# Kernel tuning notes

Hardware: AMD Instinct MI355X
Metric: run time of the kernel (lower is better)

Reference implementation:

```python
import jax, jax.numpy as jnp
import numpy as np

B, D, N = 8, 512, 4096
HEADS, DH = 8, 64
HID = HEADS * DH  # 512
SCALE = DH ** -0.5


def setup_inputs() -> dict:
    key = jax.random.key(0)
    k0, k1, k2, k3 = jax.random.split(key, 4)
    x = jax.random.normal(k0, (B, D, N), dtype=jnp.float32)
    w_qkv = jax.random.normal(k1, (3 * HID, D), dtype=jnp.float32) * 0.02
    w_out = jax.random.normal(k2, (D, HID), dtype=jnp.float32) * 0.02
    b_out = jax.random.normal(k3, (D,), dtype=jnp.float32) * 0.02
    g = jnp.ones((1, D, 1), dtype=jnp.float32)
    return {"x": x, "w_qkv": w_qkv, "w_out": w_out, "b_out": b_out, "g": g}


def reference(x, w_qkv, w_out, b_out, g):
    # 1x1 Conv1d (no bias) == channel matmul: [b, 3*HID, n]
    qkv = jnp.einsum('od,bdn->bon', w_qkv, x)
    q, k, v = jnp.split(qkv, 3, axis=1)
    # b (h c) n -> b h c n
    q = q.reshape(B, HEADS, DH, N)
    k = k.reshape(B, HEADS, DH, N)
    v = v.reshape(B, HEADS, DH, N)
    q = jax.nn.softmax(q, axis=2) * SCALE  # softmax over feature dim d
    k = jax.nn.softmax(k, axis=3)          # softmax over sequence dim n
    context = jnp.einsum('bhdn,bhen->bhde', k, v)   # [b,h,d,e]
    out = jnp.einsum('bhde,bhdn->bhen', context, q)  # [b,h,e,n]
    out = out.reshape(B, HID, N)
    # 1x1 Conv1d with bias
    y = jnp.einsum('oh,bhn->bon', w_out, out) + b_out[None, :, None]
    # RMSNorm: F.normalize(y, dim=1) * g * sqrt(D)
    norm = jnp.sqrt(jnp.sum(y * y, axis=1, keepdims=True))
    y = y / jnp.maximum(norm, 1e-12) * g * jnp.asarray(D, y.dtype) ** 0.5
    return y
```

## Files before the change

kernel.cpp:

```cpp
#include <hip/hip_runtime.h>
#include <math.h>

#define B 8
#define D 512
#define N 4096
#define HEADS 8
#define DH 64
#define HID 512
#define O3 1536
#define KDIM 512
#define SCALE 0.125f
#define SQRT_D 22.62741699796952f

typedef __attribute__((ext_vector_type(4))) float f32x4;
typedef __attribute__((ext_vector_type(8))) short bf16x8;

static __device__ __forceinline__ unsigned short f2bf(float f) {
    unsigned int u = __float_as_uint(f);
    unsigned int r = (u + 0x7fffu + ((u >> 16) & 1u)) >> 16;
    return (unsigned short)r;
}

static __device__ __forceinline__ float bf2f(unsigned short u) {
    return __uint_as_float((unsigned int)u << 16);
}

static __device__ __forceinline__ void gload_lds16(const void* g, void* l) {
    __builtin_amdgcn_global_load_lds(
        (const __attribute__((address_space(1))) unsigned int*)g,
        (__attribute__((address_space(3))) unsigned int*)l, 16, 0, 0);
}

__global__ __launch_bounds__(256) void cvt_w(const float* __restrict__ w,
                                             unsigned short* __restrict__ wb) {
    int i = (blockIdx.x * 256 + threadIdx.x) * 4;
    float4 v = *(const float4*)(w + i);
    __align__(8) unsigned short o[4] = {f2bf(v.x), f2bf(v.y), f2bf(v.z), f2bf(v.w)};
    *(uint2*)(wb + i) = *(const uint2*)o;
}

__global__ __launch_bounds__(256) void transpose_x(const float* __restrict__ x,
                                                   unsigned short* __restrict__ xT) {
    __shared__ float tile[64][65];
    const int n0 = blockIdx.x * 64, d0 = blockIdx.y * 64, b = blockIdx.z;
    const float* xb = x + (size_t)b * D * N;
    unsigned short* xTb = xT + (size_t)b * N * KDIM;
    const int t = threadIdx.x;
    const int r = t >> 4, c4 = (t & 15) * 4;
#pragma unroll
    for (int i = 0; i < 4; ++i) {
        int row = r + i * 16;
        float4 v = *(const float4*)(xb + (size_t)(d0 + row) * N + n0 + c4);
        tile[row][c4 + 0] = v.x;
        tile[row][c4 + 1] = v.y;
        tile[row][c4 + 2] = v.z;
        tile[row][c4 + 3] = v.w;
    }
    __syncthreads();
#pragma unroll
    for (int pass = 0; pass < 2; ++pass) {
        int orow = (t >> 3) + pass * 32;
        int oc = (t & 7) * 8;
        __align__(16) unsigned short o[8];
#pragma unroll
        for (int e = 0; e < 8; ++e) o[e] = f2bf(tile[oc + e][orow]);
        *(uint4*)(xTb + (size_t)(n0 + orow) * KDIM + d0 + oc) = *(const uint4*)o;
    }
}

#define GEMM_CORE(A_PTR, BT_PTR, ACC)                                              \
    __shared__ __align__(16) unsigned short As[128 * 64];                          \
    __shared__ __align__(16) unsigned short Bs[128 * 64];                          \
    const int t = threadIdx.x;                                                     \
    const int lane = t & 63;                                                       \
    const int wid = t >> 6;                                                        \
    const int wm = wid >> 1, wn = wid & 1;                                         \
    int prow[4], coff[4];                                                          \
    _Pragma("unroll") for (int i = 0; i < 4; ++i) {                                \
        int p = i * 4096 + t * 16;                                                 \
        int pr = p >> 7;                                                           \
        int pc = (p >> 4) & 7;                                                     \
        prow[i] = pr;                                                              \
        coff[i] = (pc ^ (pr & 7)) * 8;                                             \
    }                                                                              \
    int aoff[4][2], boff[4][2];                                                    \
    _Pragma("unroll") for (int m = 0; m < 4; ++m) {                                \
        int arow = wm * 64 + m * 16 + (lane & 15);                                 \
        int brow = wn * 64 + m * 16 + (lane & 15);                                 \
        _Pragma("unroll") for (int s = 0; s < 2; ++s) {                            \
            int chunk = s * 4 + (lane >> 4);                                       \
            aoff[m][s] = arow * 128 + ((chunk ^ (arow & 7)) << 4);                 \
            boff[m][s] = brow * 128 + ((chunk ^ (brow & 7)) << 4);                 \
        }                                                                          \
    }                                                                              \
    f32x4 ACC[4][4] = {};                                                          \
    for (int k0 = 0; k0 < KDIM; k0 += 64) {                                        \
        _Pragma("unroll") for (int i = 0; i < 4; ++i)                              \
            gload_lds16(A_PTR + (size_t)(row0 + prow[i]) * KDIM + k0 + coff[i],    \
                        (char*)As + i * 4096 + t * 16);                            \
        _Pragma("unroll") for (int i = 0; i < 4; ++i)                              \
            gload_lds16(BT_PTR + (size_t)(col0 + prow[i]) * KDIM + k0 + coff[i],   \
                        (char*)Bs + i * 4096 + t * 16);                            \
        __syncthreads();                                                           \
        bf16x8 af[4][2], bfr[4][2];                                                \
        _Pragma("unroll") for (int m = 0; m < 4; ++m)                              \
            _Pragma("unroll") for (int s = 0; s < 2; ++s) {                        \
                af[m][s] = *(const bf16x8*)((const char*)As + aoff[m][s]);         \
                bfr[m][s] = *(const bf16x8*)((const char*)Bs + boff[m][s]);        \
            }                                                                      \
        _Pragma("unroll") for (int s = 0; s < 2; ++s)                              \
            _Pragma("unroll") for (int m = 0; m < 4; ++m)                          \
                _Pragma("unroll") for (int n = 0; n < 4; ++n)                      \
                    ACC[m][n] = __builtin_amdgcn_mfma_f32_16x16x32_bf16(           \
                        af[m][s], bfr[n][s], ACC[m][n], 0, 0, 0);                  \
        __syncthreads();                                                           \
    }

__global__ __launch_bounds__(256) void gemm_kv(const unsigned short* __restrict__ Aw,
                                               const unsigned short* __restrict__ BTall,
                                               unsigned short* __restrict__ kvall) {
    const int b = blockIdx.z;
    const unsigned short* A = Aw;
    const unsigned short* BT = BTall + (size_t)b * N * KDIM;
    unsigned short* C = kvall + (size_t)b * 1024 * N;
    const int row0 = blockIdx.y * 128;
    const int col0 = blockIdx.x * 128;
    GEMM_CORE(A, BT, acc)
#pragma unroll
    for (int m = 0; m < 4; ++m) {
        int row_b = row0 + wm * 64 + m * 16 + (lane >> 4) * 4;
#pragma unroll
        for (int n = 0; n < 4; ++n) {
            int col = col0 + wn * 64 + n * 16 + (lane & 15);
#pragma unroll
            for (int r = 0; r < 4; ++r)
                C[(size_t)(row_b + r) * N + col] = f2bf(acc[m][n][r]);
        }
    }
}

__global__ __launch_bounds__(256) void gemm_q_sm(const unsigned short* __restrict__ Aw,
                                                 const unsigned short* __restrict__ BTall,
                                                 unsigned short* __restrict__ qT) {
    const int b = blockIdx.z;
    const unsigned short* A = Aw;
    const unsigned short* BT = BTall + (size_t)b * N * KDIM;
    const int row0 = blockIdx.y * 128;
    const int col0 = blockIdx.x * 128;
    GEMM_CORE(A, BT, acc)
    const int h = blockIdx.y * 2 + wm;
    const int g = lane >> 4;
#pragma unroll
    for (int nf = 0; nf < 4; ++nf) {
        float mx = -1e30f;
#pragma unroll
        for (int m = 0; m < 4; ++m)
#pragma unroll
            for (int r = 0; r < 4; ++r) mx = fmaxf(mx, acc[m][nf][r]);
        mx = fmaxf(mx, __shfl_xor(mx, 16));
        mx = fmaxf(mx, __shfl_xor(mx, 32));
        float e[16];
        float s = 0.f;
#pragma unroll
        for (int m = 0; m < 4; ++m)
#pragma unroll
            for (int r = 0; r < 4; ++r) {
                e[m * 4 + r] = __expf(acc[m][nf][r] - mx);
                s += e[m * 4 + r];
            }
        s += __shfl_xor(s, 16);
        s += __shfl_xor(s, 32);
        float rs = SCALE / s;
        int n = col0 + wn * 64 + nf * 16 + (lane & 15);
        unsigned short* dst = qT + ((size_t)b * N + n) * KDIM + h * 64 + g * 4;
#pragma unroll
        for (int m = 0; m < 4; ++m) {
            __align__(8) unsigned short o4[4] = {f2bf(e[m * 4 + 0] * rs), f2bf(e[m * 4 + 1] * rs),
                                                 f2bf(e[m * 4 + 2] * rs), f2bf(e[m * 4 + 3] * rs)};
            *(uint2*)(dst + m * 16) = *(const uint2*)o4;
        }
    }
}

__global__ __launch_bounds__(256) void context_mfma3(const unsigned short* __restrict__ kvb,
                                                     float* __restrict__ ctx,
                                                     float* __restrict__ ksum) {
    const int ch = blockIdx.x, h = blockIdx.y, b = blockIdx.z;
    const int K0 = ch * 512;
    const unsigned short* kbase = kvb + ((size_t)b * 1024 + h * DH) * (size_t)N + K0;
    const unsigned short* vbase = kvb + ((size_t)b * 1024 + 512 + h * DH) * (size_t)N + K0;

    __shared__ __align__(16) unsigned short Ks[64 * 64];
    __shared__ __align__(16) unsigned short Vs[64 * 64];

    const int t = threadIdx.x;
    const int lane = t & 63;
    const int wv = t >> 6;

    const int kr = t >> 2;
    const int kc = (t & 3) * 16;
    const int kchunk0 = kc >> 3;
    const int kdst0 = kr * 128 + (((kchunk0 + 0) ^ (kr & 7)) << 4);
    const int kdst1 = kr * 128 + (((kchunk0 + 1) ^ (kr & 7)) << 4);

    int vrow[2], vcoff[2];
#pragma unroll
    for (int i = 0; i < 2; ++i) {
        int p = i * 4096 + t * 16;
        int pr = p >> 7;
        int pc = (p >> 4) & 7;
        vrow[i] = pr;
        vcoff[i] = (pc ^ (pr & 7)) * 8;
    }

    const int ar = wv * 16 + (lane & 15);
    int aoff[2], boff[4][2];
#pragma unroll
    for (int s = 0; s < 2; ++s) {
        int chunk = s * 4 + (lane >> 4);
        aoff[s] = ar * 128 + ((chunk ^ (ar & 7)) << 4);
#pragma unroll
        for (int nf = 0; nf < 4; ++nf) {
            int br = nf * 16 + (lane & 15);
            boff[nf][s] = br * 128 + ((chunk ^ (br & 7)) << 4);
        }
    }

    bf16x8 ones;
#pragma unroll
    for (int j = 0; j < 8; ++j) ones[j] = (short)0x3F80;

    f32x4 acc[4] = {};
    f32x4 accs = {};

    for (int k0 = 0; k0 < 512; k0 += 64) {
#pragma unroll
        for (int i = 0; i < 2; ++i)
            gload_lds16(vbase + (size_t)vrow[i] * N + k0 + vcoff[i],
                        (char*)Vs + i * 4096 + t * 16);
        __align__(16) unsigned short raw[16];
        *(uint4*)raw = *(const uint4*)(kbase + (size_t)kr * N + k0 + kc);
        *(uint4*)(raw + 8) = *(const uint4*)(kbase + (size_t)kr * N + k0 + kc + 8);
        __align__(16) unsigned short o[16];
#pragma unroll
        for (int j = 0; j < 16; ++j) o[j] = f2bf(__expf(bf2f(raw[j])));
        *(uint4*)((char*)Ks + kdst0) = *(const uint4*)o;
        *(uint4*)((char*)Ks + kdst1) = *(const uint4*)(o + 8);
        __syncthreads();

        bf16x8 av[2], bv[4][2];
#pragma unroll
        for (int s = 0; s < 2; ++s) {
            av[s] = *(const bf16x8*)((const char*)Ks + aoff[s]);
#pragma unroll
            for (int nf = 0; nf < 4; ++nf)
                bv[nf][s] = *(const bf16x8*)((const char*)Vs + boff[nf][s]);
        }
#pragma unroll
        for (int s = 0; s < 2; ++s) {
#pragma unroll
            for (int nf = 0; nf < 4; ++nf)
                acc[nf] = __builtin_amdgcn_mfma_f32_16x16x32_bf16(av[s], bv[nf][s], acc[nf], 0, 0, 0);
            accs = __builtin_amdgcn_mfma_f32_16x16x32_bf16(av[s], ones, accs, 0, 0, 0);
        }
        __syncthreads();
    }

    float* cbase = ctx + ((size_t)(b * HEADS + h)) * DH * DH;
    const int drow = wv * 16 + (lane >> 4) * 4;
#pragma unroll
    for (int nf = 0; nf < 4; ++nf) {
        int e = nf * 16 + (lane & 15);
#pragma unroll
        for (int rr = 0; rr < 4; ++rr)
            atomicAdd(&cbase[(drow + rr) * DH + e], acc[nf][rr]);
    }
    if ((lane & 15) == 0) {
#pragma unroll
        for (int rr = 0; rr < 4; ++rr)
            atomicAdd(&ksum[b * 512 + h * DH + drow + rr], accs[rr]);
    }
}

__global__ __launch_bounds__(256) void fold_wout3(const float* __restrict__ w_out,
                                                  const float* __restrict__ ctx,
                                                  const float* __restrict__ ksum,
                                                  unsigned short* __restrict__ w2) {
    const int ot = blockIdx.x, h = blockIdx.y, b = blockIdx.z;
    __shared__ __align__(16) unsigned short As[128 * 64];
    __shared__ __align__(16) unsigned short Bs[64 * 64];
    const int t = threadIdx.x;
    const int lane = t & 63;
    const int wv = t >> 6;

#pragma unroll
    for (int i = 0; i < 8; ++i) {
        int lin = t + i * 256;
        int r = lin >> 4;
        int c4 = (lin & 15) * 4;
        float4 v = *(const float4*)(w_out + (size_t)(ot * 128 + r) * HID + h * 64 + c4);
        __align__(8) unsigned short o4[4] = {f2bf(v.x), f2bf(v.y), f2bf(v.z), f2bf(v.w)};
        int chunk = c4 >> 3;
        int off = (c4 & 7) * 2;
        *(uint2*)((char*)As + r * 128 + ((chunk ^ (r & 7)) << 4) + off) = *(const uint2*)o4;
    }
    const float* cb = ctx + ((size_t)(b * HEADS + h)) * DH * DH;
    const float* ks = ksum + b * 512 + h * 64;
#pragma unroll
    for (int i = 0; i < 4; ++i) {
        int lin = t + i * 256;
        int r = lin >> 4;
        int c4 = (lin & 15) * 4;
        float inv = 1.0f / ks[r];
        float4 v = *(const float4*)(cb + (size_t)r * DH + c4);
        __align__(8) unsigned short o4[4] = {f2bf(v.x * inv), f2bf(v.y * inv),
                                             f2bf(v.z * inv), f2bf(v.w * inv)};
        int chunk = c4 >> 3;
        int off = (c4 & 7) * 2;
        *(uint2*)((char*)Bs + r * 128 + ((chunk ^ (r & 7)) << 4) + off) = *(const uint2*)o4;
    }
    __syncthreads();

    f32x4 acc[2][4] = {};
#pragma unroll
    for (int s = 0; s < 2; ++s) {
        int chunk = s * 4 + (lane >> 4);
        bf16x8 bf[4];
#pragma unroll
        for (int nf = 0; nf < 4; ++nf) {
            int brow = nf * 16 + (lane & 15);
            bf[nf] = *(const bf16x8*)((const char*)Bs + brow * 128 + ((chunk ^ (brow & 7)) << 4));
        }
#pragma unroll
        for (int mm = 0; mm < 2; ++mm) {
            int arow = (wv * 2 + mm) * 16 + (lane & 15);
            bf16x8 a = *(const bf16x8*)((const char*)As + arow * 128 + ((chunk ^ (arow & 7)) << 4));
#pragma unroll
            for (int nf = 0; nf < 4; ++nf)
                acc[mm][nf] = __builtin_amdgcn_mfma_f32_16x16x32_bf16(a, bf[nf], acc[mm][nf], 0, 0, 0);
        }
    }

#pragma unroll
    for (int mm = 0; mm < 2; ++mm) {
        int o_base = ot * 128 + (wv * 2 + mm) * 16 + (lane >> 4) * 4;
#pragma unroll
        for (int nf = 0; nf < 4; ++nf) {
            int d = nf * 16 + (lane & 15);
#pragma unroll
            for (int rr = 0; rr < 4; ++rr)
                w2[((size_t)(b * D) + o_base + rr) * D + h * 64 + d] = f2bf(acc[mm][nf][rr]);
        }
    }
}

__global__ __launch_bounds__(256) void gemm_y(const unsigned short* __restrict__ w2all,
                                              const unsigned short* __restrict__ qTall,
                                              const float* __restrict__ bias,
                                              float* __restrict__ yall,
                                              float* __restrict__ colsum) {
    const int b = blockIdx.z;
    const unsigned short* A = w2all + (size_t)b * D * D;
    const unsigned short* BT = qTall + (size_t)b * N * KDIM;
    float* y = yall + (size_t)b * D * N;
    const int row0 = blockIdx.y * 128;
    const int col0 = blockIdx.x * 128;
    GEMM_CORE(A, BT, acc)

    float csum[4] = {0.f, 0.f, 0.f, 0.f};
#pragma unroll
    for (int m = 0; m < 4; ++m) {
        int row_b = row0 + wm * 64 + m * 16 + (lane >> 4) * 4;
#pragma unroll
        for (int r = 0; r < 4; ++r) {
            float bv = bias[row_b + r];
#pragma unroll
            for (int n = 0; n < 4; ++n) {
                int col = col0 + wn * 64 + n * 16 + (lane & 15);
                float e = acc[m][n][r] + bv;
                y[(size_t)(row_b + r) * N + col] = e;
                csum[n] += e * e;
            }
        }
    }
#pragma unroll
    for (int n = 0; n < 4; ++n) {
        csum[n] += __shfl_xor(csum[n], 16);
        csum[n] += __shfl_xor(csum[n], 32);
    }
    if (lane < 16) {
#pragma unroll
        for (int n = 0; n < 4; ++n) {
            int col = col0 + wn * 64 + n * 16 + lane;
            atomicAdd(&colsum[b * N + col], csum[n]);
        }
    }
}

__global__ __launch_bounds__(256) void colprep(float* __restrict__ cs) {
    int i = blockIdx.x * 256 + threadIdx.x;
    float v = cs[i];
    cs[i] = SQRT_D / fmaxf(sqrtf(v), 1e-12f);
}

__global__ __launch_bounds__(256) void rmsnorm4(float4* __restrict__ y,
                                                const float4* __restrict__ rinv,
                                                const float* __restrict__ g) {
    const size_t total = (size_t)B * D * N / 4;
    for (size_t i = blockIdx.x * 256 + threadIdx.x; i < total; i += 524288) {
        int b = (int)(i >> 19);
        int rem = (int)(i & 524287);
        int o = rem >> 10;
        int n4 = rem & 1023;
        float4 v = y[i];
        float4 rv = rinv[b * 1024 + n4];
        float go = g[o];
        v.x *= rv.x * go;
        v.y *= rv.y * go;
        v.z *= rv.z * go;
        v.w *= rv.w * go;
        y[i] = v;
    }
}

extern "C" void kernel_launch(void* const* d_in, const int* in_sizes, int n_in,
                              void* d_out, int out_size, void* d_ws, size_t ws_size,
                              hipStream_t stream) {
    const float* x = (const float*)d_in[0];
    const float* w_qkv = (const float*)d_in[1];
    const float* w_out = (const float*)d_in[2];
    const float* b_out = (const float*)d_in[3];
    const float* g = (const float*)d_in[4];
    float* out = (float*)d_out;

    unsigned short* kvb = (unsigned short*)d_ws;
    float* ctx = (float*)(kvb + (size_t)B * 1024 * N);
    float* ksum = ctx + (size_t)B * HEADS * DH * DH;
    float* colsum = ksum + B * 512;
    unsigned short* w2 = (unsigned short*)(colsum + B * N);
    unsigned short* wqb = w2 + (size_t)B * D * D;
    unsigned short* xT = wqb + (size_t)O3 * KDIM;
    unsigned short* qT = xT + (size_t)B * N * KDIM;

    hipMemsetAsync(ctx, 0,
                   ((size_t)B * HEADS * DH * DH + B * 512 + B * N) * sizeof(float), stream);

    cvt_w<<<dim3(O3 * KDIM / 1024), 256, 0, stream>>>(w_qkv, wqb);
    transpose_x<<<dim3(N / 64, D / 64, B), 256, 0, stream>>>(x, xT);

    gemm_q_sm<<<dim3(N / 128, HID / 128, B), 256, 0, stream>>>(wqb, xT, qT);
    gemm_kv<<<dim3(N / 128, 8, B), 256, 0, stream>>>(wqb + (size_t)HID * KDIM, xT, kvb);

    context_mfma3<<<dim3(8, HEADS, B), 256, 0, stream>>>(kvb, ctx, ksum);
    fold_wout3<<<dim3(4, HEADS, B), 256, 0, stream>>>(w_out, ctx, ksum, w2);

    gemm_y<<<dim3(N / 128, D / 128, B), 256, 0, stream>>>(w2, qT, b_out, out, colsum);

    colprep<<<dim3(B * N / 256), 256, 0, stream>>>(colsum);
    rmsnorm4<<<dim3(2048), 256, 0, stream>>>((float4*)out, (const float4*)colsum, g);
}
```

Before: 172.2 us.

## Double-buffer GEMM LDS tiles and merge Q and KV projection GEMMs

Makes the shared GEMM core double-buffered in LDS: it prefetches the next K tile while computing on the current one, with one barrier per iteration instead of two. It also merges the separate Q-softmax and KV projection GEMM launches into one gemm_qkv kernel whose blocks pick the epilogue from blockIdx.y. The aim is to hide global-to-LDS latency and to drop a launch plus tail effects. In exchange LDS use per block doubles to 64KB, which can lower occupancy.

```diff
diff --git a/kernel.cpp b/kernel.cpp
--- a/kernel.cpp
+++ b/kernel.cpp
@@ -68,9 +68,17 @@
     }
 }
 
-#define GEMM_CORE(A_PTR, BT_PTR, ACC)                                              \
-    __shared__ __align__(16) unsigned short As[128 * 64];                          \
-    __shared__ __align__(16) unsigned short Bs[128 * 64];                          \
+#define STAGE_AB(A_PTR, BT_PTR, BUFOFF, KOFF)                                      \
+    _Pragma("unroll") for (int i = 0; i < 4; ++i)                                  \
+        gload_lds16(A_PTR + (size_t)(row0 + prow[i]) * KDIM + (KOFF) + coff[i],    \
+                    (char*)As + (BUFOFF) + i * 4096 + t * 16);                     \
+    _Pragma("unroll") for (int i = 0; i < 4; ++i)                                  \
+        gload_lds16(BT_PTR + (size_t)(col0 + prow[i]) * KDIM + (KOFF) + coff[i],   \
+                    (char*)Bs + (BUFOFF) + i * 4096 + t * 16);
+
+#define GEMM_CORE_DB(A_PTR, BT_PTR, ACC)                                           \
+    __shared__ __align__(16) unsigned short As[2 * 128 * 64];                      \
+    __shared__ __align__(16) unsigned short Bs[2 * 128 * 64];                      \
     const int t = threadIdx.x;                                                     \
     const int lane = t & 63;                                                       \
     const int wid = t >> 6;                                                        \
@@ -94,19 +102,18 @@
         }                                                                          \
     }                                                                              \
     f32x4 ACC[4][4] = {};                                                          \
-    for (int k0 = 0; k0 < KDIM; k0 += 64) {                                        \
-        _Pragma("unroll") for (int i = 0; i < 4; ++i)                              \
-            gload_lds16(A_PTR + (size_t)(row0 + prow[i]) * KDIM + k0 + coff[i],    \
-                        (char*)As + i * 4096 + t * 16);                            \
-        _Pragma("unroll") for (int i = 0; i < 4; ++i)                              \
-            gload_lds16(BT_PTR + (size_t)(col0 + prow[i]) * KDIM + k0 + coff[i],   \
-                        (char*)Bs + i * 4096 + t * 16);                            \
-        __syncthreads();                                                           \
+    { STAGE_AB(A_PTR, BT_PTR, 0, 0) }                                              \
+    __syncthreads();                                                               \
+    for (int kt = 0; kt < 8; ++kt) {                                               \
+        if (kt < 7) {                                                              \
+            STAGE_AB(A_PTR, BT_PTR, ((kt + 1) & 1) * 16384, (kt + 1) * 64)         \
+        }                                                                          \
+        const int bo = (kt & 1) * 16384;                                           \
         bf16x8 af[4][2], bfr[4][2];                                                \
         _Pragma("unroll") for (int m = 0; m < 4; ++m)                              \
             _Pragma("unroll") for (int s = 0; s < 2; ++s) {                        \
-                af[m][s] = *(const bf16x8*)((const char*)As + aoff[m][s]);         \
-                bfr[m][s] = *(const bf16x8*)((const char*)Bs + boff[m][s]);        \
+                af[m][s] = *(const bf16x8*)((const char*)As + bo + aoff[m][s]);    \
+                bfr[m][s] = *(const bf16x8*)((const char*)Bs + bo + boff[m][s]);   \
             }                                                                      \
         _Pragma("unroll") for (int s = 0; s < 2; ++s)                              \
             _Pragma("unroll") for (int m = 0; m < 4; ++m)                          \
@@ -116,68 +123,64 @@
         __syncthreads();                                                           \
     }
 
-__global__ __launch_bounds__(256) void gemm_kv(const unsigned short* __restrict__ Aw,
-                                               const unsigned short* __restrict__ BTall,
-                                               unsigned short* __restrict__ kvall) {
-    const int b = blockIdx.z;
-    const unsigned short* A = Aw;
-    const unsigned short* BT = BTall + (size_t)b * N * KDIM;
-    unsigned short* C = kvall + (size_t)b * 1024 * N;
-    const int row0 = blockIdx.y * 128;
-    const int col0 = blockIdx.x * 128;
-    GEMM_CORE(A, BT, acc)
-#pragma unroll
-    for (int m = 0; m < 4; ++m) {
-        int row_b = row0 + wm * 64 + m * 16 + (lane >> 4) * 4;
-#pragma unroll
-        for (int n = 0; n < 4; ++n) {
-            int col = col0 + wn * 64 + n * 16 + (lane & 15);
-#pragma unroll
-            for (int r = 0; r < 4; ++r)
-                C[(size_t)(row_b + r) * N + col] = f2bf(acc[m][n][r]);
-        }
-    }
-}
-
-__global__ __launch_bounds__(256) void gemm_q_sm(const unsigned short* __restrict__ Aw,
-                                                 const unsigned short* __restrict__ BTall,
-                                                 unsigned short* __restrict__ qT) {
+__global__ __launch_bounds__(256) void gemm_qkv(const unsigned short* __restrict__ Aw,
+                                                const unsigned short* __restrict__ BTall,
+                                                unsigned short* __restrict__ qT,
+                                                unsigned short* __restrict__ kvall) {
     const int b = blockIdx.z;
     const unsigned short* A = Aw;
     const unsigned short* BT = BTall + (size_t)b * N * KDIM;
     const int row0 = blockIdx.y * 128;
     const int col0 = blockIdx.x * 128;
-    GEMM_CORE(A, BT, acc)
-    const int h = blockIdx.y * 2 + wm;
-    const int g = lane >> 4;
-#pragma unroll
-    for (int nf = 0; nf < 4; ++nf) {
-        float mx = -1e30f;
-#pragma unroll
-        for (int m = 0; m < 4; ++m)
-#pragma unroll
-            for (int r = 0; r < 4; ++r) mx = fmaxf(mx, acc[m][nf][r]);
-        mx = fmaxf(mx, __shfl_xor(mx, 16));
-        mx = fmaxf(mx, __shfl_xor(mx, 32));
-        float e[16];
-        float s = 0.f;
-#pragma unroll
-        for (int m = 0; m < 4; ++m)
-#pragma unroll
-            for (int r = 0; r < 4; ++r) {
-                e[m * 4 + r] = __expf(acc[m][nf][r] - mx);
-                s += e[m * 4 + r];
+    GEMM_CORE_DB(A, BT, acc)
+
+    if (blockIdx.y < 4) {
+        const int h = blockIdx.y * 2 + wm;
+        const int g = lane >> 4;
+#pragma unroll
+        for (int nf = 0; nf < 4; ++nf) {
+            float mx = -1e30f;
+#pragma unroll
+            for (int m = 0; m < 4; ++m)
+#pragma unroll
+                for (int r = 0; r < 4; ++r) mx = fmaxf(mx, acc[m][nf][r]);
+            mx = fmaxf(mx, __shfl_xor(mx, 16));
+            mx = fmaxf(mx, __shfl_xor(mx, 32));
+            float e[16];
+            float s = 0.f;
+#pragma unroll
+            for (int m = 0; m < 4; ++m)
+#pragma unroll
+                for (int r = 0; r < 4; ++r) {
+                    e[m * 4 + r] = __expf(acc[m][nf][r] - mx);
+                    s += e[m * 4 + r];
+                }
+            s += __shfl_xor(s, 16);
+            s += __shfl_xor(s, 32);
+            float rs = SCALE / s;
+            int n = col0 + wn * 64 + nf * 16 + (lane & 15);
+            unsigned short* dst = qT + ((size_t)b * N + n) * KDIM + h * 64 + g * 4;
+#pragma unroll
+            for (int m = 0; m < 4; ++m) {
+                __align__(8) unsigned short o4[4] = {
+                    f2bf(e[m * 4 + 0] * rs), f2bf(e[m * 4 + 1] * rs),
+                    f2bf(e[m * 4 + 2] * rs), f2bf(e[m * 4 + 3] * rs)};
+                *(uint2*)(dst + m * 16) = *(const uint2*)o4;
             }
-        s += __shfl_xor(s, 16);
-        s += __shfl_xor(s, 32);
-        float rs = SCALE / s;
-        int n = col0 + wn * 64 + nf * 16 + (lane & 15);
-        unsigned short* dst = qT + ((size_t)b * N + n) * KDIM + h * 64 + g * 4;
+        }
+    } else {
+        unsigned short* C = kvall + (size_t)b * 1024 * N;
+        const int rbase = row0 - 512;
 #pragma unroll
         for (int m = 0; m < 4; ++m) {
-            __align__(8) unsigned short o4[4] = {f2bf(e[m * 4 + 0] * rs), f2bf(e[m * 4 + 1] * rs),
-                                                 f2bf(e[m * 4 + 2] * rs), f2bf(e[m * 4 + 3] * rs)};
-            *(uint2*)(dst + m * 16) = *(const uint2*)o4;
+            int row_b = rbase + wm * 64 + m * 16 + (lane >> 4) * 4;
+#pragma unroll
+            for (int n = 0; n < 4; ++n) {
+                int col = col0 + wn * 64 + n * 16 + (lane & 15);
+#pragma unroll
+                for (int r = 0; r < 4; ++r)
+                    C[(size_t)(row_b + r) * N + col] = f2bf(acc[m][n][r]);
+            }
         }
     }
 }
@@ -365,7 +368,7 @@
     float* y = yall + (size_t)b * D * N;
     const int row0 = blockIdx.y * 128;
     const int col0 = blockIdx.x * 128;
-    GEMM_CORE(A, BT, acc)
+    GEMM_CORE_DB(A, BT, acc)
 
     float csum[4] = {0.f, 0.f, 0.f, 0.f};
 #pragma unroll
@@ -448,8 +451,7 @@
     cvt_w<<<dim3(O3 * KDIM / 1024), 256, 0, stream>>>(w_qkv, wqb);
     transpose_x<<<dim3(N / 64, D / 64, B), 256, 0, stream>>>(x, xT);
 
-    gemm_q_sm<<<dim3(N / 128, HID / 128, B), 256, 0, stream>>>(wqb, xT, qT);
-    gemm_kv<<<dim3(N / 128, 8, B), 256, 0, stream>>>(wqb + (size_t)HID * KDIM, xT, kvb);
+    gemm_qkv<<<dim3(N / 128, O3 / 128, B), 256, 0, stream>>>(wqb, xT, qT, kvb);
 
     context_mfma3<<<dim3(8, HEADS, B), 256, 0, stream>>>(kvb, ctx, ksum);
     fold_wout3<<<dim3(4, HEADS, B), 256, 0, stream>>>(w_out, ctx, ksum, w2);
```

Result: no change. 169.2 us (-1.7%).
